# Kernel tuning notes

Hardware: AMD Instinct MI355X
Metric: run time of the kernel (lower is better)

## Reference

```python
import jax, jax.numpy as jnp
import numpy as np

B, L, H = 2, 2048, 2048
NH, D = 16, 128          # num_heads, head_dim
MLP = 4 * H              # mlp_hidden_dim = int(hidden_size * mlp_ratio)


def setup_inputs() -> dict:
    key = jax.random.key(0)
    ks = jax.random.split(key, 8)
    x = jax.random.normal(ks[0], (B, L, H), jnp.float32)
    vec = jax.random.normal(ks[1], (B, H), jnp.float32)
    pe = jax.random.normal(ks[2], (B, 1, L, D // 2, 2, 2), jnp.float32)
    # Modulation(dim, is_double=False): Linear(H, 3H)
    mod_w = 0.02 * jax.random.normal(ks[3], (3 * H, H), jnp.float32)
    mod_b = jnp.zeros((3 * H,), jnp.float32)
    # linear1: Linear(H, 3H + MLP)
    lin1_w = 0.02 * jax.random.normal(ks[4], (3 * H + MLP, H), jnp.float32)
    lin1_b = jnp.zeros((3 * H + MLP,), jnp.float32)
    # linear2: Linear(H + MLP, H)
    lin2_w = 0.02 * jax.random.normal(ks[5], (H, H + MLP), jnp.float32)
    lin2_b = jnp.zeros((H,), jnp.float32)
    # QKNorm: RMSNorm scales over head_dim
    q_scale = jnp.ones((D,), jnp.float32)
    k_scale = jnp.ones((D,), jnp.float32)
    return dict(x=x, vec=vec, pe=pe, mod_w=mod_w, mod_b=mod_b,
                lin1_w=lin1_w, lin1_b=lin1_b, lin2_w=lin2_w, lin2_b=lin2_b,
                q_scale=q_scale, k_scale=k_scale)


def _layernorm(x, eps=1e-6):
    mu = jnp.mean(x, axis=-1, keepdims=True)
    var = jnp.mean((x - mu) ** 2, axis=-1, keepdims=True)
    return (x - mu) * jax.lax.rsqrt(var + eps)


def _rmsnorm(x, scale, eps=1e-6):
    return x * jax.lax.rsqrt(jnp.mean(x * x, axis=-1, keepdims=True) + eps) * scale


def _apply_rope(t, pe):
    # t: [B, NH, L, D]; pe: [B, 1, L, D//2, 2, 2]
    t_ = t.reshape(*t.shape[:-1], D // 2, 1, 2)
    out = pe[..., 0] * t_[..., 0] + pe[..., 1] * t_[..., 1]  # [B, NH, L, D//2, 2]
    return out.reshape(*t.shape)


def reference(x, vec, pe, mod_w, mod_b, lin1_w, lin1_b, lin2_w, lin2_b, q_scale, k_scale):
    # Modulation: silu -> linear -> (shift, scale, gate), each [B, 1, H]
    mod = jax.nn.silu(vec) @ mod_w.T + mod_b
    shift, scale, gate = jnp.split(mod[:, None, :], 3, axis=-1)

    x_mod = (1.0 + scale) * _layernorm(x) + shift

    h = x_mod @ lin1_w.T + lin1_b            # [B, L, 3H + MLP]
    qkv, mlp = h[..., :3 * H], h[..., 3 * H:]

    # 'B L (K H D) -> K B H L D'
    qkv = qkv.reshape(B, L, 3, NH, D).transpose(2, 0, 3, 1, 4)
    q, k, v = qkv[0], qkv[1], qkv[2]

    q = _rmsnorm(q, q_scale)
    k = _rmsnorm(k, k_scale)

    q = _apply_rope(q, pe)
    k = _apply_rope(k, pe)

    # SDPA with default scale 1/sqrt(D)
    logits = jnp.einsum('bhqd,bhkd->bhqk', q, k) / jnp.sqrt(jnp.float32(D))
    probs = jax.nn.softmax(logits, axis=-1)
    attn = jnp.einsum('bhqk,bhkd->bhqd', probs, v)          # [B, NH, L, D]
    attn = attn.transpose(0, 2, 1, 3).reshape(B, L, H)      # 'B H L D -> B L (H D)'

    mlp_act = jax.nn.gelu(mlp, approximate=True)
    out = jnp.concatenate([attn, mlp_act], axis=-1) @ lin2_w.T + lin2_b
    return x + gate * out
```

## Files before the change

### kernel.cpp

```cpp
#include <hip/hip_runtime.h>

#define LSEQ 2048
#define HDIM 2048
#define NHEAD 16
#define DHEAD 128
#define N1 14336
#define NC 10240

typedef unsigned short u16;
typedef __attribute__((ext_vector_type(8))) short short8;
typedef __attribute__((ext_vector_type(4))) float f32x4;

#define ASYNC16(g, l) __builtin_amdgcn_global_load_lds( \
    (__attribute__((address_space(1))) void*)(g),        \
    (__attribute__((address_space(3))) void*)(l), 16, 0, 0)

__device__ __forceinline__ u16 f2bf(float f) {
  unsigned u = __builtin_bit_cast(unsigned, f);
  u += 0x7fffu + ((u >> 16) & 1u);
  return (u16)(u >> 16);
}
__device__ __forceinline__ float bf2f(u16 v) {
  unsigned u = ((unsigned)v) << 16;
  return __builtin_bit_cast(float, u);
}
__device__ __forceinline__ float silu_f(float x) { return x / (1.f + __expf(-x)); }
__device__ __forceinline__ float gelu_f(float x) {
  float u = 0.7978845608028654f * (x + 0.044715f * x * x * x);
  float e = __expf(2.f * u);
  float th = 1.f - 2.f / (e + 1.f);
  return 0.5f * x * (1.f + th);
}

__global__ __launch_bounds__(256) void k_mod(const float* __restrict__ vec,
                                             const float* __restrict__ mod_w,
                                             const float* __restrict__ mod_b,
                                             float* __restrict__ modv) {
  int j = blockIdx.x, t = threadIdx.x;
  const float4* wr = (const float4*)(mod_w + (size_t)j * HDIM);
  const float4* vv = (const float4*)vec;
  float s0 = 0.f, s1 = 0.f;
#pragma unroll
  for (int i = 0; i < 2; i++) {
    int idx = t + i * 256;
    float4 w = wr[idx];
    float4 a = vv[idx];
    float4 c = vv[idx + 512];
    s0 += w.x*silu_f(a.x) + w.y*silu_f(a.y) + w.z*silu_f(a.z) + w.w*silu_f(a.w);
    s1 += w.x*silu_f(c.x) + w.y*silu_f(c.y) + w.z*silu_f(c.z) + w.w*silu_f(c.w);
  }
  int lane = t & 63, wid = t >> 6;
#pragma unroll
  for (int o = 32; o; o >>= 1) { s0 += __shfl_down(s0, o, 64); s1 += __shfl_down(s1, o, 64); }
  __shared__ float red[8];
  if (!lane) { red[wid] = s0; red[4 + wid] = s1; }
  __syncthreads();
  if (!t) {
    float b_ = mod_b[j];
    modv[j] = red[0]+red[1]+red[2]+red[3] + b_;
    modv[3*HDIM + j] = red[4]+red[5]+red[6]+red[7] + b_;
  }
}

__global__ __launch_bounds__(256) void k_ln(const float* __restrict__ x,
                                            const float* __restrict__ modv,
                                            u16* __restrict__ xmod) {
  int row = blockIdx.x, t = threadIdx.x;
  int b = row >> 11;
  const float4* xr = (const float4*)(x + (size_t)row * HDIM);
  float4 v0 = xr[t], v1 = xr[t + 256];
  float sum = v0.x+v0.y+v0.z+v0.w + v1.x+v1.y+v1.z+v1.w;
  float sq  = v0.x*v0.x+v0.y*v0.y+v0.z*v0.z+v0.w*v0.w
            + v1.x*v1.x+v1.y*v1.y+v1.z*v1.z+v1.w*v1.w;
  int lane = t & 63, wid = t >> 6;
#pragma unroll
  for (int o = 32; o; o >>= 1) { sum += __shfl_down(sum, o, 64); sq += __shfl_down(sq, o, 64); }
  __shared__ float red[8];
  if (!lane) { red[wid] = sum; red[4+wid] = sq; }
  __syncthreads();
  sum = red[0]+red[1]+red[2]+red[3];
  sq  = red[4]+red[5]+red[6]+red[7];
  float mu = sum * (1.f/HDIM);
  float rstd = rsqrtf(sq * (1.f/HDIM) - mu*mu + 1e-6f);
  const float* mb = modv + b * (3*HDIM);
  u16* orow = xmod + (size_t)row * HDIM;
  float vv[8] = {v0.x,v0.y,v0.z,v0.w,v1.x,v1.y,v1.z,v1.w};
#pragma unroll
  for (int half = 0; half < 2; half++) {
    int h0 = (t + half*256) * 4;
    ushort4 o4;
    float e0 = (1.f + mb[HDIM + h0+0]) * ((vv[half*4+0]-mu)*rstd) + mb[h0+0];
    float e1 = (1.f + mb[HDIM + h0+1]) * ((vv[half*4+1]-mu)*rstd) + mb[h0+1];
    float e2 = (1.f + mb[HDIM + h0+2]) * ((vv[half*4+2]-mu)*rstd) + mb[h0+2];
    float e3 = (1.f + mb[HDIM + h0+3]) * ((vv[half*4+3]-mu)*rstd) + mb[h0+3];
    o4.x = f2bf(e0); o4.y = f2bf(e1); o4.z = f2bf(e2); o4.w = f2bf(e3);
    *(ushort4*)(orow + h0) = o4;
  }
}

__global__ __launch_bounds__(256) void k_cvt(const float4* __restrict__ src,
                                             ushort4* __restrict__ dst, int n4) {
  int i = blockIdx.x * 256 + threadIdx.x;
  int stride = gridDim.x * 256;
  for (; i < n4; i += stride) {
    float4 v = src[i];
    ushort4 o;
    o.x = f2bf(v.x); o.y = f2bf(v.y); o.z = f2bf(v.z); o.w = f2bf(v.w);
    dst[i] = o;
  }
}

__global__ __launch_bounds__(256, 2) void k_gemm1(const u16* __restrict__ A,
                                                  const u16* __restrict__ Bw,
                                                  const float* __restrict__ bias,
                                                  u16* __restrict__ qkv,
                                                  u16* __restrict__ cat) {
  const int K = HDIM;
  const int NB = N1 / 128;
  int bid = blockIdx.x;
  int bm = bid / NB, bn = bid % NB;
  int t = threadIdx.x, wave = t >> 6, lane = t & 63;
  int wm = wave >> 1, wn = wave & 1;
  __shared__ u16 As[128 * 32];
  __shared__ u16 Bs[128 * 32];
  const f32x4 fzero = {0.f, 0.f, 0.f, 0.f};
  f32x4 acc[4][4];
#pragma unroll
  for (int i = 0; i < 4; i++)
#pragma unroll
    for (int j2 = 0; j2 < 4; j2++) acc[i][j2] = fzero;
  const u16* Ab = A + (size_t)bm * 128 * K;
  const u16* Bb = Bw + (size_t)bn * 128 * K;
  int r4 = lane >> 2, c4 = lane & 3;
  int fm = lane & 15, fk = (lane >> 4) * 8;
  for (int k0 = 0; k0 < K; k0 += 32) {
#pragma unroll
    for (int i = 0; i < 2; i++) {
      int row = wave*32 + i*16;
      ASYNC16(Ab + (size_t)(row + r4)*K + k0 + c4*8, &As[row*32]);
      ASYNC16(Bb + (size_t)(row + r4)*K + k0 + c4*8, &Bs[row*32]);
    }
    __syncthreads();
    short8 af[4], bfr[4];
#pragma unroll
    for (int mt = 0; mt < 4; mt++)
      af[mt] = *(const short8*)&As[(wm*64 + mt*16 + fm)*32 + fk];
#pragma unroll
    for (int nt = 0; nt < 4; nt++)
      bfr[nt] = *(const short8*)&Bs[(wn*64 + nt*16 + fm)*32 + fk];
#pragma unroll
    for (int mt = 0; mt < 4; mt++)
#pragma unroll
      for (int nt = 0; nt < 4; nt++)
        acc[mt][nt] = __builtin_amdgcn_mfma_f32_16x16x32_bf16(af[mt], bfr[nt], acc[mt][nt], 0, 0, 0);
    __syncthreads();
  }
  int rbase = bm*128 + wm*64;
  int cbase = bn*128 + wn*64;
#pragma unroll
  for (int nt = 0; nt < 4; nt++) {
    int col = cbase + nt*16 + fm;
    float bv = bias[col];
    bool isqkv = (col < 3*HDIM);
#pragma unroll
    for (int mt = 0; mt < 4; mt++) {
#pragma unroll
      for (int rr = 0; rr < 4; rr++) {
        int row = rbase + mt*16 + (lane>>4)*4 + rr;
        float v = acc[mt][nt][rr] + bv;
        if (isqkv) qkv[(size_t)row*(3*HDIM) + col] = f2bf(v);
        else       cat[(size_t)row*NC + HDIM + (col - 3*HDIM)] = f2bf(gelu_f(v));
      }
    }
  }
}

__global__ __launch_bounds__(256, 2) void k_gemm2(const u16* __restrict__ A,
                                                  const u16* __restrict__ Bw,
                                                  const float* __restrict__ bias,
                                                  const float* __restrict__ xres,
                                                  const float* __restrict__ modv,
                                                  float* __restrict__ out) {
  const int K = NC;
  const int NB = HDIM / 128;
  int bid = blockIdx.x;
  int bm = bid / NB, bn = bid % NB;
  int t = threadIdx.x, wave = t >> 6, lane = t & 63;
  int wm = wave >> 1, wn = wave & 1;
  __shared__ u16 As[128 * 32];
  __shared__ u16 Bs[128 * 32];
  const f32x4 fzero = {0.f, 0.f, 0.f, 0.f};
  f32x4 acc[4][4];
#pragma unroll
  for (int i = 0; i < 4; i++)
#pragma unroll
    for (int j2 = 0; j2 < 4; j2++) acc[i][j2] = fzero;
  const u16* Ab = A + (size_t)bm * 128 * K;
  const u16* Bb = Bw + (size_t)bn * 128 * K;
  int r4 = lane >> 2, c4 = lane & 3;
  int fm = lane & 15, fk = (lane >> 4) * 8;
  for (int k0 = 0; k0 < K; k0 += 32) {
#pragma unroll
    for (int i = 0; i < 2; i++) {
      int row = wave*32 + i*16;
      ASYNC16(Ab + (size_t)(row + r4)*K + k0 + c4*8, &As[row*32]);
      ASYNC16(Bb + (size_t)(row + r4)*K + k0 + c4*8, &Bs[row*32]);
    }
    __syncthreads();
    short8 af[4], bfr[4];
#pragma unroll
    for (int mt = 0; mt < 4; mt++)
      af[mt] = *(const short8*)&As[(wm*64 + mt*16 + fm)*32 + fk];
#pragma unroll
    for (int nt = 0; nt < 4; nt++)
      bfr[nt] = *(const short8*)&Bs[(wn*64 + nt*16 + fm)*32 + fk];
#pragma unroll
    for (int mt = 0; mt < 4; mt++)
#pragma unroll
      for (int nt = 0; nt < 4; nt++)
        acc[mt][nt] = __builtin_amdgcn_mfma_f32_16x16x32_bf16(af[mt], bfr[nt], acc[mt][nt], 0, 0, 0);
    __syncthreads();
  }
  int rbase = bm*128 + wm*64;
  int cbase = bn*128 + wn*64;
  int b = (bm*128) >> 11;
#pragma unroll
  for (int nt = 0; nt < 4; nt++) {
    int col = cbase + nt*16 + fm;
    float bv = bias[col];
    float g = modv[b*(3*HDIM) + 2*HDIM + col];
#pragma unroll
    for (int mt = 0; mt < 4; mt++) {
#pragma unroll
      for (int rr = 0; rr < 4; rr++) {
        int row = rbase + mt*16 + (lane>>4)*4 + rr;
        size_t idx = (size_t)row*HDIM + col;
        out[idx] = xres[idx] + g * (acc[mt][nt][rr] + bv);
      }
    }
  }
}

__global__ __launch_bounds__(128) void k_qk(const u16* __restrict__ qkv,
                                            const float* __restrict__ pe,
                                            const float* __restrict__ q_scale,
                                            const float* __restrict__ k_scale,
                                            u16* __restrict__ Q, u16* __restrict__ Ko) {
  int bid = blockIdx.x;
  int l = bid & (LSEQ-1);
  int h = (bid >> 11) & (NHEAD-1);
  int b = bid >> 15;
  int d = threadIdx.x;
  const u16* base = qkv + ((size_t)(b*LSEQ + l)) * (3*HDIM);
  float qv = bf2f(base[h*DHEAD + d]);
  float kv = bf2f(base[HDIM + h*DHEAD + d]);
  float sq = qv*qv, sk = kv*kv;
  int lane = d & 63, wid = d >> 6;
#pragma unroll
  for (int o = 32; o; o >>= 1) { sq += __shfl_down(sq, o, 64); sk += __shfl_down(sk, o, 64); }
  __shared__ float red[4];
  __shared__ float qn[128], kn[128];
  if (!lane) { red[wid] = sq; red[2+wid] = sk; }
  __syncthreads();
  float rq = rsqrtf((red[0]+red[1]) * (1.f/DHEAD) + 1e-6f);
  float rk = rsqrtf((red[2]+red[3]) * (1.f/DHEAD) + 1e-6f);
  qn[d] = qv * rq * q_scale[d];
  kn[d] = kv * rk * k_scale[d];
  __syncthreads();
  int p = d >> 1, j = d & 1;
  const float2 pp = *(const float2*)(pe + (((size_t)(b*LSEQ + l))*64 + p)*4 + j*2);
  float qo = pp.x * qn[2*p] + pp.y * qn[2*p+1];
  float ko = pp.x * kn[2*p] + pp.y * kn[2*p+1];
  size_t oidx = (((size_t)(b*NHEAD + h))*LSEQ + l)*DHEAD + d;
  Q[oidx]  = f2bf(qo);
  Ko[oidx] = f2bf(ko);
}

__global__ __launch_bounds__(256) void k_vt(const u16* __restrict__ qkv, u16* __restrict__ Vt) {
  int bid = blockIdx.x;
  int lt = bid & 31, h = (bid >> 5) & 15, b = bid >> 9;
  __shared__ u16 tile[64][132];
  int t = threadIdx.x;
#pragma unroll
  for (int it = 0; it < 8; it++) {
    int idx = it*1024 + t*4;
    int li = idx >> 7, di = idx & 127;
    const u16* src = qkv + ((size_t)(b*LSEQ + lt*64 + li))*(3*HDIM) + 2*HDIM + h*DHEAD + di;
    ushort4 v = *(const ushort4*)src;
    *(ushort4*)&tile[li][di] = v;
  }
  __syncthreads();
  u16* dst = Vt + ((size_t)(b*NHEAD + h))*DHEAD*LSEQ + lt*64;
#pragma unroll
  for (int it = 0; it < 32; it++) {
    int idx = it*256 + t;
    int lo = idx & 63, dd = idx >> 6;
    dst[(size_t)dd*LSEQ + lo] = tile[lo][dd];
  }
}

#define ATT_SCALE 0.08838834764831845f
__global__ __launch_bounds__(256, 2) void k_attn(const u16* __restrict__ Q,
                                                 const u16* __restrict__ Kc,
                                                 const u16* __restrict__ Vt,
                                                 u16* __restrict__ cat) {
  __shared__ u16 Qs[64*128];
  __shared__ u16 Ks[64*128];
  __shared__ u16 Vs[128*64];
  __shared__ u16 Ps[64*72];
  int bid = blockIdx.x;
  int qt = bid & 31, h = (bid >> 5) & 15, b = bid >> 9;
  int t = threadIdx.x, wave = t >> 6, lane = t & 63;
  int fm = lane & 15, fq = lane >> 4;
  int r8 = lane >> 3, c8 = lane & 7;
  const u16* Qg = Q  + (((size_t)(b*NHEAD + h))*LSEQ + qt*64) * DHEAD;
  const u16* Kg = Kc + ((size_t)(b*NHEAD + h))*LSEQ * DHEAD;
  const u16* Vg = Vt + ((size_t)(b*NHEAD + h))*DHEAD*LSEQ;
#pragma unroll
  for (int i = 0; i < 4; i++) {
    int row = wave*16 + i*4;
    ASYNC16(Qg + (size_t)(row + fq)*DHEAD + fm*8, &Qs[row*DHEAD]);
  }
  const f32x4 fzero = {0.f, 0.f, 0.f, 0.f};
  f32x4 o[8];
#pragma unroll
  for (int i = 0; i < 8; i++) o[i] = fzero;
  float m_i[4], l_i[4];
#pragma unroll
  for (int r = 0; r < 4; r++) { m_i[r] = -1e30f; l_i[r] = 0.f; }
  for (int kt = 0; kt < 32; kt++) {
    const u16* Kt_ = Kg + (size_t)kt*64*DHEAD;
    const u16* Vt_ = Vg + kt*64;
#pragma unroll
    for (int i = 0; i < 4; i++) {
      int row = wave*16 + i*4;
      ASYNC16(Kt_ + (size_t)(row + fq)*DHEAD + fm*8, &Ks[row*DHEAD]);
      int vrow = wave*32 + i*8;
      ASYNC16(Vt_ + (size_t)(vrow + r8)*LSEQ + c8*8, &Vs[vrow*64]);
    }
    __syncthreads();
    f32x4 s[4];
#pragma unroll
    for (int nt = 0; nt < 4; nt++) s[nt] = fzero;
#pragma unroll
    for (int ks = 0; ks < 4; ks++) {
      short8 aq = *(const short8*)&Qs[(wave*16 + fm)*DHEAD + ks*32 + fq*8];
#pragma unroll
      for (int nt = 0; nt < 4; nt++) {
        short8 bk = *(const short8*)&Ks[(nt*16 + fm)*DHEAD + ks*32 + fq*8];
        s[nt] = __builtin_amdgcn_mfma_f32_16x16x32_bf16(aq, bk, s[nt], 0, 0, 0);
      }
    }
    float rowm[4];
#pragma unroll
    for (int r = 0; r < 4; r++)
      rowm[r] = fmaxf(fmaxf(s[0][r], s[1][r]), fmaxf(s[2][r], s[3][r])) * ATT_SCALE;
#pragma unroll
    for (int r = 0; r < 4; r++) {
#pragma unroll
      for (int o2 = 8; o2 >= 1; o2 >>= 1)
        rowm[r] = fmaxf(rowm[r], __shfl_xor(rowm[r], o2, 64));
    }
    float alpha[4];
#pragma unroll
    for (int r = 0; r < 4; r++) {
      float mnew = fmaxf(m_i[r], rowm[r]);
      alpha[r] = __expf(m_i[r] - mnew);
      m_i[r] = mnew;
    }
    float rs[4] = {0.f, 0.f, 0.f, 0.f};
#pragma unroll
    for (int nt = 0; nt < 4; nt++)
#pragma unroll
      for (int r = 0; r < 4; r++) {
        float p = __expf(s[nt][r] * ATT_SCALE - m_i[r]);
        s[nt][r] = p;
        rs[r] += p;
      }
#pragma unroll
    for (int r = 0; r < 4; r++) {
#pragma unroll
      for (int o2 = 8; o2 >= 1; o2 >>= 1) rs[r] += __shfl_xor(rs[r], o2, 64);
      l_i[r] = l_i[r] * alpha[r] + rs[r];
    }
#pragma unroll
    for (int i = 0; i < 8; i++)
#pragma unroll
      for (int r = 0; r < 4; r++) o[i][r] *= alpha[r];
#pragma unroll
    for (int nt = 0; nt < 4; nt++)
#pragma unroll
      for (int r = 0; r < 4; r++)
        Ps[(wave*16 + fq*4 + r)*72 + nt*16 + fm] = f2bf(s[nt][r]);
    __syncthreads();
#pragma unroll
    for (int ks = 0; ks < 2; ks++) {
      short8 ap = *(const short8*)&Ps[(wave*16 + fm)*72 + ks*32 + fq*8];
#pragma unroll
      for (int nt = 0; nt < 8; nt++) {
        short8 bv = *(const short8*)&Vs[(nt*16 + fm)*64 + ks*32 + fq*8];
        o[nt] = __builtin_amdgcn_mfma_f32_16x16x32_bf16(ap, bv, o[nt], 0, 0, 0);
      }
    }
    __syncthreads();
  }
#pragma unroll
  for (int nt = 0; nt < 8; nt++) {
#pragma unroll
    for (int r = 0; r < 4; r++) {
      int l = qt*64 + wave*16 + fq*4 + r;
      int d = nt*16 + fm;
      float v = o[nt][r] / l_i[r];
      cat[((size_t)(b*LSEQ + l))*NC + h*DHEAD + d] = f2bf(v);
    }
  }
}

extern "C" void kernel_launch(void* const* d_in, const int* in_sizes, int n_in,
                              void* d_out, int out_size, void* d_ws, size_t ws_size,
                              hipStream_t stream) {
  const float* x       = (const float*)d_in[0];
  const float* vec     = (const float*)d_in[1];
  const float* pe      = (const float*)d_in[2];
  const float* mod_w   = (const float*)d_in[3];
  const float* mod_b   = (const float*)d_in[4];
  const float* lin1_w  = (const float*)d_in[5];
  const float* lin1_b  = (const float*)d_in[6];
  const float* lin2_w  = (const float*)d_in[7];
  const float* lin2_b  = (const float*)d_in[8];
  const float* q_scale = (const float*)d_in[9];
  const float* k_scale = (const float*)d_in[10];
  char* ws = (char*)d_ws;

  float* modv = (float*)(ws + 0);
  u16* xmod  = (u16*)(ws + 65536ULL);
  u16* qkv   = (u16*)(ws + 16842752ULL);
  u16* cat   = (u16*)(ws + 67174400ULL);
  u16* w2    = (u16*)(ws + 151060480ULL);
  u16* w1    = (u16*)(ws + 193003520ULL);
  u16* Qb    = (u16*)(ws + 193003520ULL);
  u16* Kb    = (u16*)(ws + 209780736ULL);
  u16* Vtb   = (u16*)(ws + 226557952ULL);

  k_mod<<<dim3(3*HDIM), dim3(256), 0, stream>>>(vec, mod_w, mod_b, modv);
  k_cvt<<<dim3(4096), dim3(256), 0, stream>>>((const float4*)lin1_w, (ushort4*)w1, (N1*HDIM)/4);
  k_cvt<<<dim3(4096), dim3(256), 0, stream>>>((const float4*)lin2_w, (ushort4*)w2, (HDIM*NC)/4);
  k_ln<<<dim3(4096), dim3(256), 0, stream>>>(x, modv, xmod);
  k_gemm1<<<dim3(32*112), dim3(256), 0, stream>>>(xmod, w1, lin1_b, qkv, cat);
  k_qk<<<dim3(65536), dim3(128), 0, stream>>>(qkv, pe, q_scale, k_scale, Qb, Kb);
  k_vt<<<dim3(1024), dim3(256), 0, stream>>>(qkv, Vtb);
  k_attn<<<dim3(1024), dim3(256), 0, stream>>>(Qb, Kb, Vtb, cat);
  k_gemm2<<<dim3(32*16), dim3(256), 0, stream>>>(cat, w2, lin2_b, x, modv, (float*)d_out);
}
```

Baseline: 1.213 ms.

## Stage GEMM1 epilogue in LDS, vectorize QK norm, double-buffer attention K/V

GEMM1 now writes its tile into a padded shared buffer and stores it to global memory in coalesced 16-byte rows instead of scattered 2-byte stores. The Q/K RMSNorm+RoPE kernel handles a whole token per block with 8-element vector loads and shuffle reductions, which removes shared-memory round trips and cuts the block count. The attention kernel keeps Q in registers and double-buffers the K/V tiles so the next tile loads while the current one is computed. It also replaces the per-wave P barrier with a waitcnt. That last step relies on each wave reading only its own P rows, which holds here but is fragile.

```diff
diff --git a/kernel.cpp b/kernel.cpp
--- a/kernel.cpp
+++ b/kernel.cpp
@@ -121,8 +121,9 @@
   int bm = bid / NB, bn = bid % NB;
   int t = threadIdx.x, wave = t >> 6, lane = t & 63;
   int wm = wave >> 1, wn = wave & 1;
-  __shared__ u16 As[128 * 32];
-  __shared__ u16 Bs[128 * 32];
+  __shared__ u16 S[128 * 136];
+  u16* As = S;
+  u16* Bs = S + 4096;
   const f32x4 fzero = {0.f, 0.f, 0.f, 0.f};
   f32x4 acc[4][4];
 #pragma unroll
@@ -132,7 +133,7 @@
   const u16* Ab = A + (size_t)bm * 128 * K;
   const u16* Bb = Bw + (size_t)bn * 128 * K;
   int r4 = lane >> 2, c4 = lane & 3;
-  int fm = lane & 15, fk = (lane >> 4) * 8;
+  int fm = lane & 15, fk = (lane >> 4) * 8, fq = lane >> 4;
   for (int k0 = 0; k0 < K; k0 += 32) {
 #pragma unroll
     for (int i = 0; i < 2; i++) {
@@ -155,23 +156,34 @@
         acc[mt][nt] = __builtin_amdgcn_mfma_f32_16x16x32_bf16(af[mt], bfr[nt], acc[mt][nt], 0, 0, 0);
     __syncthreads();
   }
-  int rbase = bm*128 + wm*64;
-  int cbase = bn*128 + wn*64;
+  bool ismlp = (bn >= 48);
 #pragma unroll
   for (int nt = 0; nt < 4; nt++) {
-    int col = cbase + nt*16 + fm;
-    float bv = bias[col];
-    bool isqkv = (col < 3*HDIM);
+    int col_l = wn*64 + nt*16 + fm;
+    float bv = bias[bn*128 + col_l];
 #pragma unroll
     for (int mt = 0; mt < 4; mt++) {
 #pragma unroll
       for (int rr = 0; rr < 4; rr++) {
-        int row = rbase + mt*16 + (lane>>4)*4 + rr;
+        int row_l = wm*64 + mt*16 + fq*4 + rr;
         float v = acc[mt][nt][rr] + bv;
-        if (isqkv) qkv[(size_t)row*(3*HDIM) + col] = f2bf(v);
-        else       cat[(size_t)row*NC + HDIM + (col - 3*HDIM)] = f2bf(gelu_f(v));
-      }
-    }
+        if (ismlp) v = gelu_f(v);
+        S[row_l*136 + col_l] = f2bf(v);
+      }
+    }
+  }
+  __syncthreads();
+  int c = (t & 15) * 8;
+  int rq = t >> 4;
+#pragma unroll
+  for (int p = 0; p < 8; p++) {
+    int r_l = p*16 + rq;
+    short8 v = *(const short8*)&S[r_l*136 + c];
+    int row_g = bm*128 + r_l;
+    if (!ismlp)
+      *(short8*)(qkv + (size_t)row_g*(3*HDIM) + bn*128 + c) = v;
+    else
+      *(short8*)(cat + (size_t)row_g*NC + HDIM + (bn-48)*128 + c) = v;
   }
 }
 
@@ -241,39 +253,53 @@
   }
 }
 
-__global__ __launch_bounds__(128) void k_qk(const u16* __restrict__ qkv,
+__global__ __launch_bounds__(256) void k_qk(const u16* __restrict__ qkv,
                                             const float* __restrict__ pe,
                                             const float* __restrict__ q_scale,
                                             const float* __restrict__ k_scale,
                                             u16* __restrict__ Q, u16* __restrict__ Ko) {
   int bid = blockIdx.x;
   int l = bid & (LSEQ-1);
-  int h = (bid >> 11) & (NHEAD-1);
-  int b = bid >> 15;
-  int d = threadIdx.x;
-  const u16* base = qkv + ((size_t)(b*LSEQ + l)) * (3*HDIM);
-  float qv = bf2f(base[h*DHEAD + d]);
-  float kv = bf2f(base[HDIM + h*DHEAD + d]);
-  float sq = qv*qv, sk = kv*kv;
-  int lane = d & 63, wid = d >> 6;
-#pragma unroll
-  for (int o = 32; o; o >>= 1) { sq += __shfl_down(sq, o, 64); sk += __shfl_down(sk, o, 64); }
-  __shared__ float red[4];
-  __shared__ float qn[128], kn[128];
-  if (!lane) { red[wid] = sq; red[2+wid] = sk; }
-  __syncthreads();
-  float rq = rsqrtf((red[0]+red[1]) * (1.f/DHEAD) + 1e-6f);
-  float rk = rsqrtf((red[2]+red[3]) * (1.f/DHEAD) + 1e-6f);
-  qn[d] = qv * rq * q_scale[d];
-  kn[d] = kv * rk * k_scale[d];
-  __syncthreads();
-  int p = d >> 1, j = d & 1;
-  const float2 pp = *(const float2*)(pe + (((size_t)(b*LSEQ + l))*64 + p)*4 + j*2);
-  float qo = pp.x * qn[2*p] + pp.y * qn[2*p+1];
-  float ko = pp.x * kn[2*p] + pp.y * kn[2*p+1];
-  size_t oidx = (((size_t)(b*NHEAD + h))*LSEQ + l)*DHEAD + d;
-  Q[oidx]  = f2bf(qo);
-  Ko[oidx] = f2bf(ko);
+  int b = bid >> 11;
+  int t = threadIdx.x;
+  int h = t >> 4;
+  int dc = (t & 15) * 8;
+  const u16* base = qkv + (size_t)bid * (3*HDIM);
+  short8 q8 = *(const short8*)(base + h*DHEAD + dc);
+  short8 k8 = *(const short8*)(base + HDIM + h*DHEAD + dc);
+  float qf[8], kf[8];
+  float sq = 0.f, sk = 0.f;
+#pragma unroll
+  for (int i = 0; i < 8; i++) {
+    qf[i] = bf2f((u16)q8[i]); kf[i] = bf2f((u16)k8[i]);
+    sq += qf[i]*qf[i]; sk += kf[i]*kf[i];
+  }
+#pragma unroll
+  for (int m = 1; m < 16; m <<= 1) { sq += __shfl_xor(sq, m, 64); sk += __shfl_xor(sk, m, 64); }
+  float rq = rsqrtf(sq * (1.f/DHEAD) + 1e-6f);
+  float rk = rsqrtf(sk * (1.f/DHEAD) + 1e-6f);
+  float4 qs0 = *(const float4*)(q_scale + dc), qs1 = *(const float4*)(q_scale + dc + 4);
+  float4 ks0 = *(const float4*)(k_scale + dc), ks1 = *(const float4*)(k_scale + dc + 4);
+  float qsc[8] = {qs0.x,qs0.y,qs0.z,qs0.w,qs1.x,qs1.y,qs1.z,qs1.w};
+  float ksc[8] = {ks0.x,ks0.y,ks0.z,ks0.w,ks1.x,ks1.y,ks1.z,ks1.w};
+  float qn[8], kn[8];
+#pragma unroll
+  for (int i = 0; i < 8; i++) { qn[i] = qf[i]*rq*qsc[i]; kn[i] = kf[i]*rk*ksc[i]; }
+  const float4* pe4 = (const float4*)pe + ((size_t)bid*64 + (dc >> 1));
+  short8 qo, ko;
+#pragma unroll
+  for (int pi = 0; pi < 4; pi++) {
+    float4 pp = pe4[pi];
+    float q0 = pp.x*qn[2*pi] + pp.y*qn[2*pi+1];
+    float q1 = pp.z*qn[2*pi] + pp.w*qn[2*pi+1];
+    float k0 = pp.x*kn[2*pi] + pp.y*kn[2*pi+1];
+    float k1 = pp.z*kn[2*pi] + pp.w*kn[2*pi+1];
+    qo[2*pi] = (short)f2bf(q0); qo[2*pi+1] = (short)f2bf(q1);
+    ko[2*pi] = (short)f2bf(k0); ko[2*pi+1] = (short)f2bf(k1);
+  }
+  size_t oidx = (((size_t)(b*NHEAD + h))*LSEQ + l)*DHEAD + dc;
+  *(short8*)(Q + oidx) = qo;
+  *(short8*)(Ko + oidx) = ko;
 }
 
 __global__ __launch_bounds__(256) void k_vt(const u16* __restrict__ qkv, u16* __restrict__ Vt) {
@@ -304,22 +330,28 @@
                                                  const u16* __restrict__ Kc,
                                                  const u16* __restrict__ Vt,
                                                  u16* __restrict__ cat) {
-  __shared__ u16 Qs[64*128];
-  __shared__ u16 Ks[64*128];
-  __shared__ u16 Vs[128*64];
-  __shared__ u16 Ps[64*72];
+  __shared__ u16 Ks[2*64*128];
+  __shared__ u16 Vs[2*128*64];
+  __shared__ u16 Ps[64*88];
   int bid = blockIdx.x;
-  int qt = bid & 31, h = (bid >> 5) & 15, b = bid >> 9;
+  int bh = bid & 31, qt = bid >> 5;
+  int h = bh & 15, b = bh >> 4;
   int t = threadIdx.x, wave = t >> 6, lane = t & 63;
   int fm = lane & 15, fq = lane >> 4;
   int r8 = lane >> 3, c8 = lane & 7;
   const u16* Qg = Q  + (((size_t)(b*NHEAD + h))*LSEQ + qt*64) * DHEAD;
   const u16* Kg = Kc + ((size_t)(b*NHEAD + h))*LSEQ * DHEAD;
   const u16* Vg = Vt + ((size_t)(b*NHEAD + h))*DHEAD*LSEQ;
+  short8 aq[4];
+#pragma unroll
+  for (int ks = 0; ks < 4; ks++)
+    aq[ks] = *(const short8*)(Qg + (size_t)(wave*16 + fm)*DHEAD + ks*32 + fq*8);
 #pragma unroll
   for (int i = 0; i < 4; i++) {
     int row = wave*16 + i*4;
-    ASYNC16(Qg + (size_t)(row + fq)*DHEAD + fm*8, &Qs[row*DHEAD]);
+    ASYNC16(Kg + (size_t)(row + fq)*DHEAD + fm*8, &Ks[row*DHEAD]);
+    int vrow = wave*32 + i*8;
+    ASYNC16(Vg + (size_t)(vrow + r8)*LSEQ + c8*8, &Vs[vrow*64]);
   }
   const f32x4 fzero = {0.f, 0.f, 0.f, 0.f};
   f32x4 o[8];
@@ -329,26 +361,31 @@
 #pragma unroll
   for (int r = 0; r < 4; r++) { m_i[r] = -1e30f; l_i[r] = 0.f; }
   for (int kt = 0; kt < 32; kt++) {
-    const u16* Kt_ = Kg + (size_t)kt*64*DHEAD;
-    const u16* Vt_ = Vg + kt*64;
-#pragma unroll
-    for (int i = 0; i < 4; i++) {
-      int row = wave*16 + i*4;
-      ASYNC16(Kt_ + (size_t)(row + fq)*DHEAD + fm*8, &Ks[row*DHEAD]);
-      int vrow = wave*32 + i*8;
-      ASYNC16(Vt_ + (size_t)(vrow + r8)*LSEQ + c8*8, &Vs[vrow*64]);
-    }
+    int cur = kt & 1;
     __syncthreads();
+    if (kt < 31) {
+      int off = (cur ^ 1) * 8192;
+      const u16* Kt_ = Kg + (size_t)(kt+1)*64*DHEAD;
+      const u16* Vt_ = Vg + (kt+1)*64;
+#pragma unroll
+      for (int i = 0; i < 4; i++) {
+        int row = wave*16 + i*4;
+        ASYNC16(Kt_ + (size_t)(row + fq)*DHEAD + fm*8, &Ks[off + row*DHEAD]);
+        int vrow = wave*32 + i*8;
+        ASYNC16(Vt_ + (size_t)(vrow + r8)*LSEQ + c8*8, &Vs[off + vrow*64]);
+      }
+    }
+    const u16* Kb = &Ks[cur*8192];
+    const u16* Vb = &Vs[cur*8192];
     f32x4 s[4];
 #pragma unroll
     for (int nt = 0; nt < 4; nt++) s[nt] = fzero;
 #pragma unroll
     for (int ks = 0; ks < 4; ks++) {
-      short8 aq = *(const short8*)&Qs[(wave*16 + fm)*DHEAD + ks*32 + fq*8];
 #pragma unroll
       for (int nt = 0; nt < 4; nt++) {
-        short8 bk = *(const short8*)&Ks[(nt*16 + fm)*DHEAD + ks*32 + fq*8];
-        s[nt] = __builtin_amdgcn_mfma_f32_16x16x32_bf16(aq, bk, s[nt], 0, 0, 0);
+        short8 bk = *(const short8*)&Kb[(nt*16 + fm)*DHEAD + ks*32 + fq*8];
+        s[nt] = __builtin_amdgcn_mfma_f32_16x16x32_bf16(aq[ks], bk, s[nt], 0, 0, 0);
       }
     }
     float rowm[4];
@@ -391,18 +428,17 @@
     for (int nt = 0; nt < 4; nt++)
 #pragma unroll
       for (int r = 0; r < 4; r++)
-        Ps[(wave*16 + fq*4 + r)*72 + nt*16 + fm] = f2bf(s[nt][r]);
-    __syncthreads();
-#pragma unroll
-    for (int ks = 0; ks < 2; ks++) {
-      short8 ap = *(const short8*)&Ps[(wave*16 + fm)*72 + ks*32 + fq*8];
+        Ps[(wave*16 + fq*4 + r)*88 + nt*16 + fm] = f2bf(s[nt][r]);
+    asm volatile("s_waitcnt lgkmcnt(0)" ::: "memory");
+#pragma unroll
+    for (int ks2 = 0; ks2 < 2; ks2++) {
+      short8 ap = *(const short8*)&Ps[(wave*16 + fm)*88 + ks2*32 + fq*8];
 #pragma unroll
       for (int nt = 0; nt < 8; nt++) {
-        short8 bv = *(const short8*)&Vs[(nt*16 + fm)*64 + ks*32 + fq*8];
+        short8 bv = *(const short8*)&Vb[(nt*16 + fm)*64 + ks2*32 + fq*8];
         o[nt] = __builtin_amdgcn_mfma_f32_16x16x32_bf16(ap, bv, o[nt], 0, 0, 0);
       }
     }
-    __syncthreads();
   }
 #pragma unroll
   for (int nt = 0; nt < 8; nt++) {
@@ -447,7 +483,7 @@
   k_cvt<<<dim3(4096), dim3(256), 0, stream>>>((const float4*)lin2_w, (ushort4*)w2, (HDIM*NC)/4);
   k_ln<<<dim3(4096), dim3(256), 0, stream>>>(x, modv, xmod);
   k_gemm1<<<dim3(32*112), dim3(256), 0, stream>>>(xmod, w1, lin1_b, qkv, cat);
-  k_qk<<<dim3(65536), dim3(128), 0, stream>>>(qkv, pe, q_scale, k_scale, Qb, Kb);
+  k_qk<<<dim3(4096), dim3(256), 0, stream>>>(qkv, pe, q_scale, k_scale, Qb, Kb);
   k_vt<<<dim3(1024), dim3(256), 0, stream>>>(qkv, Vtb);
   k_attn<<<dim3(1024), dim3(256), 0, stream>>>(Qb, Kb, Vtb, cat);
   k_gemm2<<<dim3(32*16), dim3(256), 0, stream>>>(cat, w2, lin2_b, x, modv, (float*)d_out);
```

Measured after the change: 1.185 ms. -2.3%, faster.
